# Optimization experiments

Hardware: AMD Instinct MI355X
Metric: run time of the kernel (lower is better)

Reference implementation:

```python
import jax, jax.numpy as jnp
import numpy as np

HIDDEN_DIM = 512
SCALE = float(np.sqrt(HIDDEN_DIM))  # hidden_dim ** 0.5, matches torch


def setup_inputs() -> dict:
    key = jax.random.key(0)
    ks = jax.random.split(key, 4)
    B, S, D_IN = 8, 4096, 64
    x = jax.random.normal(ks[0], (B, S, D_IN), dtype=jnp.float32)
    # Linear weights stored as [in, out] (transposed vs torch's [out, in])
    Wq = jax.random.normal(ks[1], (D_IN, HIDDEN_DIM), dtype=jnp.float32) * (1.0 / np.sqrt(D_IN))
    Wk = jax.random.normal(ks[2], (D_IN, HIDDEN_DIM), dtype=jnp.float32) * (1.0 / np.sqrt(D_IN))
    Wv = jax.random.normal(ks[3], (D_IN, HIDDEN_DIM), dtype=jnp.float32) * (1.0 / np.sqrt(D_IN))
    bq = jnp.zeros((HIDDEN_DIM,), dtype=jnp.float32)
    bk = jnp.zeros((HIDDEN_DIM,), dtype=jnp.float32)
    bv = jnp.zeros((HIDDEN_DIM,), dtype=jnp.float32)
    return {"x": x, "Wq": Wq, "bq": bq, "Wk": Wk, "bk": bk, "Wv": Wv, "bv": bv}


def reference(x, Wq, bq, Wk, bk, Wv, bv):
    # Q/K/V projections: [B, S, H]
    Q = jnp.einsum('bsd,dh->bsh', x, Wq) + bq
    K = jnp.einsum('bsd,dh->bsh', x, Wk) + bk
    V = jnp.einsum('bsd,dh->bsh', x, Wv) + bv
    # Naive single-head attention with full [B, S, S] score matrix,
    # matching the original torch math exactly.
    scores = jnp.einsum('bqh,bkh->bqk', Q, K) / SCALE
    attn = jax.nn.softmax(scores, axis=-1)
    return jnp.einsum('bqk,bkh->bqh', attn, V)
```

## Files before the change

### kernel.cpp

```cpp
#include <hip/hip_runtime.h>
#include <hip/hip_bf16.h>
#include <math.h>


#define SS 4096
#define DD 64
#define HH 512

#define CSCALE ((float)(1.4426950408889634 * 0.04419417382415922))

typedef __bf16 bf16x8 __attribute__((ext_vector_type(8)));
typedef float  f32x4  __attribute__((ext_vector_type(4)));
typedef unsigned int u32x4 __attribute__((ext_vector_type(4)));

__device__ __forceinline__ float b2f(__hip_bfloat16 v) { return __bfloat162float(v); }

__device__ __forceinline__ f32x4 mfma16(bf16x8 a, bf16x8 b, f32x4 c) {
  return __builtin_amdgcn_mfma_f32_16x16x32_bf16(a, b, c, 0, 0, 0);
}

__device__ __forceinline__ unsigned pack2(float a, float b) {
  float2 f2; f2.x = a; f2.y = b;
  __hip_bfloat162 h2 = __float22bfloat162_rn(f2);
  unsigned u; __builtin_memcpy(&u, &h2, 4);
  return u;
}

__device__ __forceinline__ float loadf(const void* p, size_t i, int isF32) {
  return isF32 ? ((const float*)p)[i] : b2f(((const __hip_bfloat16*)p)[i]);
}
__device__ __forceinline__ void load8f(const void* p, size_t i, int isF32, float* o) {
  if (isF32) {
    const float4 a = *(const float4*)((const float*)p + i);
    const float4 b = *(const float4*)((const float*)p + i + 4);
    o[0]=a.x; o[1]=a.y; o[2]=a.z; o[3]=a.w; o[4]=b.x; o[5]=b.y; o[6]=b.z; o[7]=b.w;
  } else {
    const bf16x8 v = *(const bf16x8*)((const __hip_bfloat16*)p + i);
#pragma unroll
    for (int k = 0; k < 8; ++k) { __hip_bfloat16 h; __builtin_memcpy(&h, ((const unsigned short*)&v) + k, 2); o[k] = b2f(h); }
  }
}

__global__ void dtype_probe(const void* __restrict__ Wq, int* __restrict__ flag) {
  const unsigned short* h = (const unsigned short*)Wq;
  const int lane = threadIdx.x;
  unsigned int bits = ((unsigned int)h[lane * 2]) << 16;
  float v; __builtin_memcpy(&v, &bits, 4);
  v = fabsf(v);
  if (!isfinite(v) || v > 1e10f) v = 1e10f;
  for (int off = 1; off < 64; off <<= 1) v = fmaxf(v, __shfl_xor(v, off, 64));
  if (lane == 0) *flag = (v > 1e6f) ? 1 : 0;
}

__global__ __launch_bounds__(256) void prep_kernel(
    const void* __restrict__ Wq, const void* __restrict__ Wk,
    const void* __restrict__ Wv, const void* __restrict__ bq,
    const void* __restrict__ bk, __hip_bfloat16* __restrict__ MT,
    float* __restrict__ u, float* __restrict__ w_, float* __restrict__ c_,
    __hip_bfloat16* __restrict__ wvT, const int* __restrict__ flag) {
  const int t = threadIdx.x, blk = blockIdx.x;
  const int isF32 = *flag;
  if (blk < 64) {
    __shared__ float red[256];
    const int i = blk, j = t >> 2, part = t & 3;
    float acc = 0.f, aq[8], ak[8];
    for (int c = 0; c < 16; ++c) {
      load8f(Wq, (size_t)i * HH + part * 128 + c * 8, isF32, aq);
      load8f(Wk, (size_t)j * HH + part * 128 + c * 8, isF32, ak);
#pragma unroll
      for (int k = 0; k < 8; ++k) acc = fmaf(aq[k], ak[k], acc);
    }
    red[t] = acc;
    __syncthreads();
    if (t < 64)
      MT[t * 64 + i] = __float2bfloat16(red[t*4] + red[t*4+1] + red[t*4+2] + red[t*4+3]);
  } else if (blk == 64) {
    __shared__ float pu[256], pw[256], pc[64];
    const int i = t & 63, part = t >> 6;
    float au = 0.f, aw = 0.f, v1[8], v2[8];
    for (int c = 0; c < 16; ++c) {
      load8f(Wq, (size_t)i * HH + part * 128 + c * 8, isF32, v1);
      load8f(bk, part * 128 + c * 8, isF32, v2);
#pragma unroll
      for (int k = 0; k < 8; ++k) au = fmaf(v1[k], v2[k], au);
      load8f(Wk, (size_t)i * HH + part * 128 + c * 8, isF32, v1);
      load8f(bq, part * 128 + c * 8, isF32, v2);
#pragma unroll
      for (int k = 0; k < 8; ++k) aw = fmaf(v1[k], v2[k], aw);
    }
    pu[t] = au; pw[t] = aw;
    if (t < 64) {
      float s = 0.f;
      for (int e = 0; e < 8; ++e)
        s = fmaf(loadf(bq, t * 8 + e, isF32), loadf(bk, t * 8 + e, isF32), s);
      pc[t] = s;
    }
    __syncthreads();
    if (t < 64) {
      u[t]  = pu[t] + pu[t+64] + pu[t+128] + pu[t+192];
      w_[t] = pw[t] + pw[t+64] + pw[t+128] + pw[t+192];
    }
    if (t == 0) {
      float s = 0.f;
      for (int e = 0; e < 64; ++e) s += pc[e];
      *c_ = s;
    }
  } else {
    const int base = (blk - 65) * 2048 + t;
    for (int r = 0; r < 8; ++r) {
      const int e = base + r * 256;
      const int h = e >> 6, d = e & 63;
      wvT[e] = __float2bfloat16(loadf(Wv, (size_t)d * HH + h, isF32));
    }
  }
}

__global__ __launch_bounds__(256) void proj_kernel(
    const void* __restrict__ xraw, const __hip_bfloat16* __restrict__ MT,
    const float* __restrict__ u, const float* __restrict__ w_,
    const float* __restrict__ c_, __hip_bfloat16* __restrict__ xc,
    __hip_bfloat16* __restrict__ y, float* __restrict__ qb,
    float* __restrict__ kb, __hip_bfloat16* __restrict__ xT,
    const int* __restrict__ flag) {
  __shared__ __hip_bfloat16 xs[64 * 72];
  __shared__ __hip_bfloat16 Ms[64 * 72];
  __shared__ float us[64], wl[64];
  __shared__ float cs;

  const int t = threadIdx.x;
  const int isF32 = *flag;
  {
    const int r = t >> 2, cb = (t & 3) * 16;
    *(bf16x8*)(&Ms[r * 72 + cb])     = *(const bf16x8*)(MT + r * 64 + cb);
    *(bf16x8*)(&Ms[r * 72 + cb + 8]) = *(const bf16x8*)(MT + r * 64 + cb + 8);
  }
  if (t < 64) { us[t] = u[t]; wl[t] = w_[t]; }
  if (t == 0) cs = *c_;

  const int b = blockIdx.x & 7;
  const int sbase = (blockIdx.x >> 3) * 64;
  const int rbase = b * SS + sbase;

  for (int i = 0; i < 2; ++i) {
    const int e = i * 256 + t;
    const int row = e >> 3, col = (e & 7) * 8;
    float v[8];
    load8f(xraw, (size_t)(rbase + row) * DD + col, isF32, v);
    __hip_bfloat16* dp = xs + row * 72 + col;
#pragma unroll
    for (int k = 0; k < 8; ++k) dp[k] = __float2bfloat16(v[k]);
  }
  __syncthreads();

  const int wv = t >> 6, lane = t & 63;
  const int l16 = lane & 15, quad = lane >> 4;
  const bf16x8 A0 = *(const bf16x8*)(&xs[(wv * 16 + l16) * 72 + quad * 8]);
  const bf16x8 A1 = *(const bf16x8*)(&xs[(wv * 16 + l16) * 72 + 32 + quad * 8]);
#pragma unroll
  for (int nt = 0; nt < 4; ++nt) {
    const bf16x8 B0 = *(const bf16x8*)(&Ms[(nt * 16 + l16) * 72 + quad * 8]);
    const bf16x8 B1 = *(const bf16x8*)(&Ms[(nt * 16 + l16) * 72 + 32 + quad * 8]);
    f32x4 C = (f32x4){0.f, 0.f, 0.f, 0.f};
    C = mfma16(A0, B0, C);
    C = mfma16(A1, B1, C);
#pragma unroll
    for (int r = 0; r < 4; ++r)
      y[(size_t)(rbase + wv * 16 + quad * 4 + r) * DD + nt * 16 + l16] =
          __float2bfloat16(C[r]);
  }
  if (t < 64) {
    float qa = 0.f, ka = 0.f;
    for (int d = 0; d < 64; ++d) {
      const float xv = b2f(xs[t * 72 + d]);
      qa = fmaf(xv, us[d], qa);
      ka = fmaf(xv, wl[d], ka);
    }
    qb[rbase + t] = (qa + cs) * CSCALE;
    kb[rbase + t] = ka * CSCALE;
  }
  for (int i = 0; i < 2; ++i) {
    const int e = i * 256 + t;
    const int row = e >> 3, col = (e & 7) * 8;
    *(bf16x8*)(xc + (size_t)(rbase + row) * DD + col) = *(const bf16x8*)(xs + row * 72 + col);
  }
  for (int i = 0; i < 16; ++i) {
    const int d = i * 4 + (t >> 6);
    const int sl = t & 63;
    xT[((size_t)b * DD + d) * SS + sbase + sl] = xs[sl * 72 + d];
  }
}

__global__ __launch_bounds__(256) void attn_kernel(
    const __hip_bfloat16* __restrict__ x,
    const __hip_bfloat16* __restrict__ y,
    const float* __restrict__ qb, const float* __restrict__ kb,
    const __hip_bfloat16* __restrict__ xT,
    const __hip_bfloat16* __restrict__ wvT,
    const void* __restrict__ bv_raw,
    void* __restrict__ out_raw, const int* __restrict__ flag) {
  __shared__ __hip_bfloat16 xs[2][32 * 72];
  __shared__ __hip_bfloat16 vsm[2][64 * 40];
  __shared__ float kbl[SS];
  const int tid = threadIdx.x;
  const int wv = tid >> 6, lane = tid & 63;
  const int l16 = lane & 15, quad = lane >> 4;
  const int b = blockIdx.x & 7;
  const int qt = (blockIdx.x >> 3) * 4 + wv;
  const size_t rowq = ((size_t)b << 12) + ((size_t)qt << 4);
  const int isF32 = *flag;

  const __hip_bfloat16* xb  = x  + ((size_t)b * SS) * DD;
  const __hip_bfloat16* xTb = xT + ((size_t)b * DD) * SS;
  const float* kbb = kb + ((size_t)b * SS);

  const __hip_bfloat16* yp = y + (rowq + l16) * DD + quad * 8;
  const bf16x8 Ylo = *(const bf16x8*)yp;
  const bf16x8 Yhi = *(const bf16x8*)(yp + 32);
  const float qbl = qb[rowq + l16];

  const int sxr = tid >> 3, sxc = (tid & 7) * 8;
  const int taur = (sxr & 3) + ((sxr >> 3) << 2) + (((sxr >> 2) & 1) << 4);
  const int svd = tid >> 2, svc = (tid & 3) * 8;
  const __hip_bfloat16* gx = xb + (size_t)sxr * DD + sxc;
  const __hip_bfloat16* gv = xTb + (size_t)svd * SS + svc;

#pragma unroll
  for (int j = 0; j < 4; ++j) {
    const int c = j * 256 + tid;
    *(f32x4*)(&kbl[c * 4]) = *(const f32x4*)(kbb + c * 4);
  }

  bf16x8 nx = *(const bf16x8*)gx;
  bf16x8 nv = *(const bf16x8*)gv;
  *(bf16x8*)(&xs[0][taur * 72 + sxc]) = nx;
  *(bf16x8*)(&vsm[0][svd * 40 + svc]) = nv;
  nx = *(const bf16x8*)(gx + 32 * DD);
  nv = *(const bf16x8*)(gv + 32);
  __syncthreads();

  bf16x8 onesb;
#pragma unroll
  for (int j = 0; j < 8; ++j) onesb[j] = (__bf16)1.0f;

  f32x4 O[4];
#pragma unroll
  for (int n = 0; n < 4; ++n) O[n] = (f32x4){0.f, 0.f, 0.f, 0.f};
  f32x4 Ol = (f32x4){0.f, 0.f, 0.f, 0.f};

  for (int kt = 0; kt < SS; kt += 32) {
    const int p = (kt >> 5) & 1, np = p ^ 1;
    if (kt + 32 < SS) {
      *(bf16x8*)(&xs[np][taur * 72 + sxc]) = nx;
      *(bf16x8*)(&vsm[np][svd * 40 + svc]) = nv;
      if (kt + 64 < SS) {
        nx = *(const bf16x8*)(gx + (size_t)(kt + 64) * DD);
        nv = *(const bf16x8*)(gv + (kt + 64));
      }
    }

    const bf16x8 B00 = *(const bf16x8*)(&xs[p][l16 * 72 + quad * 8]);
    const bf16x8 B01 = *(const bf16x8*)(&xs[p][l16 * 72 + 32 + quad * 8]);
    const bf16x8 B10 = *(const bf16x8*)(&xs[p][(16 + l16) * 72 + quad * 8]);
    const bf16x8 B11 = *(const bf16x8*)(&xs[p][(16 + l16) * 72 + 32 + quad * 8]);
    const bf16x8 V0 = *(const bf16x8*)(&vsm[p][l16 * 40 + quad * 8]);
    const bf16x8 V1 = *(const bf16x8*)(&vsm[p][(16 + l16) * 40 + quad * 8]);
    const bf16x8 V2 = *(const bf16x8*)(&vsm[p][(32 + l16) * 40 + quad * 8]);
    const bf16x8 V3 = *(const bf16x8*)(&vsm[p][(48 + l16) * 40 + quad * 8]);

    f32x4 S0 = (f32x4){0.f, 0.f, 0.f, 0.f};
    f32x4 S1 = (f32x4){0.f, 0.f, 0.f, 0.f};
    S0 = mfma16(B00, Ylo, S0);
    S0 = mfma16(B01, Yhi, S0);
    S1 = mfma16(B10, Ylo, S1);
    S1 = mfma16(B11, Yhi, S1);

    const f32x4 kb0 = *(const f32x4*)(&kbl[kt + quad * 8]);
    const f32x4 kb1 = *(const f32x4*)(&kbl[kt + quad * 8 + 4]);

    float p0[4], p1[4];
#pragma unroll
    for (int r = 0; r < 4; ++r) {
      p0[r] = __builtin_amdgcn_exp2f(fmaf(S0[r], CSCALE, qbl + kb0[r]));
      p1[r] = __builtin_amdgcn_exp2f(fmaf(S1[r], CSCALE, qbl + kb1[r]));
    }
    u32x4 R;
    R[0] = pack2(p0[0], p0[1]);
    R[1] = pack2(p0[2], p0[3]);
    R[2] = pack2(p1[0], p1[1]);
    R[3] = pack2(p1[2], p1[3]);
    bf16x8 Pf;
    __builtin_memcpy(&Pf, &R, 16);

    O[0] = mfma16(Pf, V0, O[0]);
    O[1] = mfma16(Pf, V1, O[1]);
    O[2] = mfma16(Pf, V2, O[2]);
    O[3] = mfma16(Pf, V3, O[3]);
    Ol = mfma16(Pf, onesb, Ol);

    __syncthreads();
  }

  float inv_l[4];
#pragma unroll
  for (int r = 0; r < 4; ++r)
    inv_l[r] = (Ol[r] > 0.f) ? 1.0f / Ol[r] : 0.f;
  __hip_bfloat16* pl = &xs[0][0] + wv * 1152;
#pragma unroll
  for (int n = 0; n < 4; ++n)
#pragma unroll
    for (int r = 0; r < 4; ++r) {
      const int row = quad * 4 + r;
      pl[row * 72 + n * 16 + l16] = __float2bfloat16(O[n][r] * inv_l[r]);
    }
  __syncthreads();
  const bf16x8 Alo = *(const bf16x8*)(pl + l16 * 72 + quad * 8);
  const bf16x8 Ahi = *(const bf16x8*)(pl + l16 * 72 + 32 + quad * 8);

  float* outf = (float*)out_raw;
  __hip_bfloat16* outb = (__hip_bfloat16*)out_raw;
#pragma unroll 4
  for (int ht = 0; ht < 32; ++ht) {
    const __hip_bfloat16* wp = wvT + (size_t)(ht * 16 + l16) * DD + quad * 8;
    const bf16x8 Wlo = *(const bf16x8*)wp;
    const bf16x8 Whi = *(const bf16x8*)(wp + 32);
    f32x4 C = (f32x4){0.f, 0.f, 0.f, 0.f};
    C = mfma16(Alo, Wlo, C);
    C = mfma16(Ahi, Whi, C);
    const float bvv = loadf(bv_raw, ht * 16 + l16, isF32);
#pragma unroll
    for (int r = 0; r < 4; ++r) {
      const size_t oidx = (rowq + quad * 4 + r) * HH + ht * 16 + l16;
      const float val = C[r] + bvv;
      if (isF32) outf[oidx] = val;
      else       outb[oidx] = __float2bfloat16(val);
    }
  }
}

extern "C" void kernel_launch(void* const* d_in, const int* in_sizes, int n_in,
                              void* d_out, int out_size, void* d_ws,
                              size_t ws_size, hipStream_t stream) {
  char* ws = (char*)d_ws;
  int*   flag = (int*)(ws + 0);
  __hip_bfloat16* MT = (__hip_bfloat16*)(ws + 1024);
  float* u    = (float*)(ws + 9216);
  float* w_   = (float*)(ws + 9728);
  float* c_   = (float*)(ws + 10240);
  __hip_bfloat16* wvT = (__hip_bfloat16*)(ws + 32768);
  __hip_bfloat16* xc  = (__hip_bfloat16*)(ws + 131072);
  __hip_bfloat16* y   = (__hip_bfloat16*)(ws + 4325376);
  float* qb = (float*)(ws + 8519680);
  float* kb = (float*)(ws + 8650752);
  __hip_bfloat16* xT = (__hip_bfloat16*)(ws + 8781824);

  dtype_probe<<<1, 64, 0, stream>>>(d_in[1], flag);
  prep_kernel<<<81, 256, 0, stream>>>(d_in[1], d_in[3], d_in[5], d_in[2],
                                      d_in[4], MT, u, w_, c_, wvT, flag);
  proj_kernel<<<512, 256, 0, stream>>>(d_in[0], MT, u, w_, c_, xc, y, qb, kb,
                                       xT, flag);
  attn_kernel<<<512, 256, 0, stream>>>(xc, y, qb, kb, xT, wvT, d_in[6], d_out,
                                       flag);
}
```

Baseline: 189.3 us.

## Split attention over key dimension with separate combine and Wv projection kernel

Adds a split-K attention kernel that divides the 4096 keys into two halves, doubling the grid to 1024 blocks and writing fp32 partial outputs and row sums to workspace. A new combine kernel sums the partials, normalizes them, and applies the Wv projection plus bias. This targets low occupancy and the long serial key loop of the single attention kernel. The cost is extra global traffic for the partial buffers (about 16MB) and one more launch. The new path is used only when the workspace is large enough.

```diff
diff --git a/kernel.cpp b/kernel.cpp
--- a/kernel.cpp
+++ b/kernel.cpp
@@ -6,6 +6,7 @@
 #define SS 4096
 #define DD 64
 #define HH 512
+#define KSPL 2048
 
 #define CSCALE ((float)(1.4426950408889634 * 0.04419417382415922))
 
@@ -187,6 +188,180 @@
     const int d = i * 4 + (t >> 6);
     const int sl = t & 63;
     xT[((size_t)b * DD + d) * SS + sbase + sl] = xs[sl * 72 + d];
+  }
+}
+
+__global__ __launch_bounds__(256) void attn_split(
+    const __hip_bfloat16* __restrict__ x,
+    const __hip_bfloat16* __restrict__ y,
+    const float* __restrict__ qb, const float* __restrict__ kb,
+    const __hip_bfloat16* __restrict__ xT,
+    float* __restrict__ Opart, float* __restrict__ lpart) {
+  __shared__ __hip_bfloat16 xs[2][32 * 72];
+  __shared__ __hip_bfloat16 vsm[2][64 * 40];
+  const int tid = threadIdx.x;
+  const int wv = tid >> 6, lane = tid & 63;
+  const int l16 = lane & 15, quad = lane >> 4;
+  const int b = blockIdx.x & 7;
+  const int ks = (blockIdx.x >> 3) & 1;
+  const int qt = (blockIdx.x >> 4) * 4 + wv;
+  const int koff = ks * KSPL;
+  const size_t rowq = ((size_t)b << 12) + ((size_t)qt << 4);
+
+  const __hip_bfloat16* xb  = x  + ((size_t)b * SS) * DD;
+  const __hip_bfloat16* xTb = xT + ((size_t)b * DD) * SS;
+  const float* kbb = kb + ((size_t)b * SS);
+
+  const __hip_bfloat16* yp = y + (rowq + l16) * DD + quad * 8;
+  const bf16x8 Ylo = *(const bf16x8*)yp;
+  const bf16x8 Yhi = *(const bf16x8*)(yp + 32);
+  const float qbl = qb[rowq + l16];
+
+  const int sxr = tid >> 3, sxc = (tid & 7) * 8;
+  const int taur = (sxr & 3) + ((sxr >> 3) << 2) + (((sxr >> 2) & 1) << 4);
+  const int svd = tid >> 2, svc = (tid & 3) * 8;
+  const __hip_bfloat16* gx = xb + (size_t)(koff + sxr) * DD + sxc;
+  const __hip_bfloat16* gv = xTb + (size_t)svd * SS + koff + svc;
+  const float* kbp = kbb + koff + quad * 8;
+
+  bf16x8 nx = *(const bf16x8*)gx;
+  bf16x8 nv = *(const bf16x8*)gv;
+  *(bf16x8*)(&xs[0][taur * 72 + sxc]) = nx;
+  *(bf16x8*)(&vsm[0][svd * 40 + svc]) = nv;
+  nx = *(const bf16x8*)(gx + 32 * DD);
+  nv = *(const bf16x8*)(gv + 32);
+  __syncthreads();
+
+  bf16x8 onesb;
+#pragma unroll
+  for (int j = 0; j < 8; ++j) onesb[j] = (__bf16)1.0f;
+
+  f32x4 O[4];
+#pragma unroll
+  for (int n = 0; n < 4; ++n) O[n] = (f32x4){0.f, 0.f, 0.f, 0.f};
+  f32x4 Ol = (f32x4){0.f, 0.f, 0.f, 0.f};
+
+  for (int kt = 0; kt < KSPL; kt += 32) {
+    const int p = (kt >> 5) & 1, np = p ^ 1;
+    if (kt + 32 < KSPL) {
+      *(bf16x8*)(&xs[np][taur * 72 + sxc]) = nx;
+      *(bf16x8*)(&vsm[np][svd * 40 + svc]) = nv;
+      if (kt + 64 < KSPL) {
+        nx = *(const bf16x8*)(gx + (size_t)(kt + 64) * DD);
+        nv = *(const bf16x8*)(gv + (kt + 64));
+      }
+    }
+    const f32x4 kb0 = *(const f32x4*)(kbp + kt);
+    const f32x4 kb1 = *(const f32x4*)(kbp + kt + 4);
+
+    const bf16x8 B00 = *(const bf16x8*)(&xs[p][l16 * 72 + quad * 8]);
+    const bf16x8 B01 = *(const bf16x8*)(&xs[p][l16 * 72 + 32 + quad * 8]);
+    const bf16x8 B10 = *(const bf16x8*)(&xs[p][(16 + l16) * 72 + quad * 8]);
+    const bf16x8 B11 = *(const bf16x8*)(&xs[p][(16 + l16) * 72 + 32 + quad * 8]);
+    const bf16x8 V0 = *(const bf16x8*)(&vsm[p][l16 * 40 + quad * 8]);
+    const bf16x8 V1 = *(const bf16x8*)(&vsm[p][(16 + l16) * 40 + quad * 8]);
+    const bf16x8 V2 = *(const bf16x8*)(&vsm[p][(32 + l16) * 40 + quad * 8]);
+    const bf16x8 V3 = *(const bf16x8*)(&vsm[p][(48 + l16) * 40 + quad * 8]);
+
+    f32x4 S0 = (f32x4){0.f, 0.f, 0.f, 0.f};
+    f32x4 S1 = (f32x4){0.f, 0.f, 0.f, 0.f};
+    S0 = mfma16(B00, Ylo, S0);
+    S0 = mfma16(B01, Yhi, S0);
+    S1 = mfma16(B10, Ylo, S1);
+    S1 = mfma16(B11, Yhi, S1);
+
+    float p0[4], p1[4];
+#pragma unroll
+    for (int r = 0; r < 4; ++r) {
+      p0[r] = __builtin_amdgcn_exp2f(fmaf(S0[r], CSCALE, qbl + kb0[r]));
+      p1[r] = __builtin_amdgcn_exp2f(fmaf(S1[r], CSCALE, qbl + kb1[r]));
+    }
+    u32x4 R;
+    R[0] = pack2(p0[0], p0[1]);
+    R[1] = pack2(p0[2], p0[3]);
+    R[2] = pack2(p1[0], p1[1]);
+    R[3] = pack2(p1[2], p1[3]);
+    bf16x8 Pf;
+    __builtin_memcpy(&Pf, &R, 16);
+
+    O[0] = mfma16(Pf, V0, O[0]);
+    O[1] = mfma16(Pf, V1, O[1]);
+    O[2] = mfma16(Pf, V2, O[2]);
+    O[3] = mfma16(Pf, V3, O[3]);
+    Ol = mfma16(Pf, onesb, Ol);
+
+    __syncthreads();
+  }
+
+  float* Op = Opart + ((size_t)ks * (SS * 8) + rowq) * 64;
+#pragma unroll
+  for (int n = 0; n < 4; ++n)
+#pragma unroll
+    for (int r = 0; r < 4; ++r)
+      Op[(size_t)(quad * 4 + r) * 64 + n * 16 + l16] = O[n][r];
+  if (l16 == 0) {
+#pragma unroll
+    for (int r = 0; r < 4; ++r)
+      lpart[(size_t)ks * (SS * 8) + rowq + quad * 4 + r] = Ol[r];
+  }
+}
+
+__global__ __launch_bounds__(256) void combine_kernel(
+    const float* __restrict__ Opart, const float* __restrict__ lpart,
+    const __hip_bfloat16* __restrict__ wvT, const void* __restrict__ bv_raw,
+    void* __restrict__ out_raw, const int* __restrict__ flag) {
+  const int tid = threadIdx.x;
+  const int wv = tid >> 6, lane = tid & 63;
+  const int l16 = lane & 15, quad = lane >> 4;
+  const size_t q0 = (size_t)blockIdx.x * 64 + (size_t)wv * 16;
+  const int isF32 = *flag;
+  const size_t NP = (size_t)SS * 8;
+
+  const float lsum = lpart[q0 + l16] + lpart[NP + q0 + l16];
+  const float linv = (lsum > 0.f) ? 1.0f / lsum : 0.f;
+
+  const float* p0 = Opart + (q0 + l16) * 64 + quad * 8;
+  const float* p1 = p0 + NP * 64;
+  float vlo[8], vhi[8];
+#pragma unroll
+  for (int j = 0; j < 8; j += 4) {
+    const float4 a = *(const float4*)(p0 + j);
+    const float4 b = *(const float4*)(p1 + j);
+    vlo[j]   = (a.x + b.x) * linv; vlo[j+1] = (a.y + b.y) * linv;
+    vlo[j+2] = (a.z + b.z) * linv; vlo[j+3] = (a.w + b.w) * linv;
+    const float4 c = *(const float4*)(p0 + 32 + j);
+    const float4 d = *(const float4*)(p1 + 32 + j);
+    vhi[j]   = (c.x + d.x) * linv; vhi[j+1] = (c.y + d.y) * linv;
+    vhi[j+2] = (c.z + d.z) * linv; vhi[j+3] = (c.w + d.w) * linv;
+  }
+  u32x4 Rlo, Rhi;
+#pragma unroll
+  for (int j = 0; j < 4; ++j) {
+    Rlo[j] = pack2(vlo[2*j], vlo[2*j+1]);
+    Rhi[j] = pack2(vhi[2*j], vhi[2*j+1]);
+  }
+  bf16x8 Alo, Ahi;
+  __builtin_memcpy(&Alo, &Rlo, 16);
+  __builtin_memcpy(&Ahi, &Rhi, 16);
+
+  float* outf = (float*)out_raw;
+  __hip_bfloat16* outb = (__hip_bfloat16*)out_raw;
+#pragma unroll 4
+  for (int ht = 0; ht < 32; ++ht) {
+    const __hip_bfloat16* wp = wvT + (size_t)(ht * 16 + l16) * DD + quad * 8;
+    const bf16x8 Wlo = *(const bf16x8*)wp;
+    const bf16x8 Whi = *(const bf16x8*)(wp + 32);
+    f32x4 C = (f32x4){0.f, 0.f, 0.f, 0.f};
+    C = mfma16(Alo, Wlo, C);
+    C = mfma16(Ahi, Whi, C);
+    const float bvv = loadf(bv_raw, ht * 16 + l16, isF32);
+#pragma unroll
+    for (int r = 0; r < 4; ++r) {
+      const size_t oidx = (q0 + quad * 4 + r) * HH + ht * 16 + l16;
+      const float val = C[r] + bvv;
+      if (isF32) outf[oidx] = val;
+      else       outb[oidx] = __float2bfloat16(val);
+    }
   }
 }
 
@@ -257,7 +432,6 @@
         nv = *(const bf16x8*)(gv + (kt + 64));
       }
     }
-
     const bf16x8 B00 = *(const bf16x8*)(&xs[p][l16 * 72 + quad * 8]);
     const bf16x8 B01 = *(const bf16x8*)(&xs[p][l16 * 72 + 32 + quad * 8]);
     const bf16x8 B10 = *(const bf16x8*)(&xs[p][(16 + l16) * 72 + quad * 8]);
@@ -352,12 +526,21 @@
   float* qb = (float*)(ws + 8519680);
   float* kb = (float*)(ws + 8650752);
   __hip_bfloat16* xT = (__hip_bfloat16*)(ws + 8781824);
+  float* Opart = (float*)(ws + 16777216);
+  float* lpart = (float*)(ws + 33554432);
+  const size_t ws_need = 33816576;
 
   dtype_probe<<<1, 64, 0, stream>>>(d_in[1], flag);
   prep_kernel<<<81, 256, 0, stream>>>(d_in[1], d_in[3], d_in[5], d_in[2],
                                       d_in[4], MT, u, w_, c_, wvT, flag);
   proj_kernel<<<512, 256, 0, stream>>>(d_in[0], MT, u, w_, c_, xc, y, qb, kb,
                                        xT, flag);
-  attn_kernel<<<512, 256, 0, stream>>>(xc, y, qb, kb, xT, wvT, d_in[6], d_out,
-                                       flag);
-}
+  if (ws_size >= ws_need) {
+    attn_split<<<1024, 256, 0, stream>>>(xc, y, qb, kb, xT, Opart, lpart);
+    combine_kernel<<<512, 256, 0, stream>>>(Opart, lpart, wvT, d_in[6], d_out,
+                                            flag);
+  } else {
+    attn_kernel<<<512, 256, 0, stream>>>(xc, y, qb, kb, xT, wvT, d_in[6],
+                                         d_out, flag);
+  }
+}
```

Measured after the change: 190.1 us. No clear change (+0.4%).
